# Kernel optimization log

Hardware: AMD Instinct MI355X
Metric: run time of the kernel (lower is better)

Reference implementation:

```python
import jax, jax.numpy as jnp
import numpy as np

H = 128  # hidden_size hard-coded in the torch module


def _lin(key, fan_in, shape):
    b = 1.0 / np.sqrt(fan_in)
    return jax.random.uniform(key, shape, minval=-b, maxval=b, dtype=jnp.float32)


def _gru_step(x, wih, bih, bhh):
    # torch GRU, single time step, h0 = 0; gate order (r, z, n)
    g = x @ wih.T + bih
    xr, xz, xn = jnp.split(g, 3, axis=-1)
    br, bz, bn = jnp.split(bhh, 3)
    r = jax.nn.sigmoid(xr + br)
    z = jax.nn.sigmoid(xz + bz)
    n = jnp.tanh(xn + r * bn)
    return (1.0 - z) * n  # h' = (1-z)*n + z*0


def _forward(x_node, x_edge, nt_w1, nt_b1, nt_w2, nt_b2, et_w, et_b,
             ngru_wih, ngru_bih, ngru_bhh, egru_wih, egru_bih, egru_bhh,
             natt_w, natt_b, eatt_w, eatt_b,
             lr_w1, lr_b1, lr_w2, lr_b2, cr_w1, cr_b1, cr_w2, cr_b2,
             mr_w1, mr_b1, mr_w2, mr_b2, pairs):
    B, N, _ = x_node.shape
    node_f = jax.nn.relu(x_node @ nt_w1 + nt_b1) @ nt_w2 + nt_b2      # [B,N,H]
    edge_f = x_edge @ et_w + et_b                                      # [B,N,N,H]
    nh = eh = None
    for _ in range(2):  # num_time_steps; GRU inputs are NOT updated in the original loop
        nh = _gru_step(node_f, ngru_wih, ngru_bih, ngru_bhh)           # [B,N,H]
        eh = _gru_step(edge_f, egru_wih, egru_bih, egru_bhh)           # [B,N,N,H]
        # --- node message pooling: attention over column index j ---
        n_col = jnp.broadcast_to(nh[:, :, None, :], eh.shape)          # aug[b,i,j] = nh[b,i]
        logits = (jnp.concatenate([n_col, eh], -1) @ natt_w)[..., 0] + natt_b[0]
        w = jax.nn.softmax(logits, axis=-1)                            # [B,N,N]
        nh = jnp.einsum('bijk,bij->bik', eh, w)                        # pooled node states
        # --- edge message pooling: 2-way attention over (row, col) node states ---
        n_row = jnp.broadcast_to(nh[:, None, :, :], eh.shape)          # [b,i,j] = nh[b,j]
        n_col = jnp.broadcast_to(nh[:, :, None, :], eh.shape)          # [b,i,j] = nh[b,i]
        l_row = (jnp.concatenate([n_row, eh], -1) @ eatt_w)[..., 0] + eatt_b[0]
        l_col = (jnp.concatenate([n_col, eh], -1) @ eatt_w)[..., 0] + eatt_b[0]
        w2 = jax.nn.softmax(jnp.stack([l_row, l_col], -1), axis=-1)    # [B,N,N,2]
        eh = w2[..., 0:1] * n_row + w2[..., 1:2] * n_col               # einsum('bijl,bijkl->bijk')
    # --- classifier inputs (aggregator = elementwise mean) ---
    i0, i1 = pairs[..., 0], pairs[..., 1]                              # [B,P]
    emb0 = jnp.take_along_axis(nh, i0[..., None], axis=1)              # [B,P,H]
    emb1 = jnp.take_along_axis(nh, i1[..., None], axis=1)
    bix = jnp.arange(B)[:, None]
    e01 = eh[bix, i0, i1]                                              # [B,P,H]
    e10 = eh[bix, i1, i0]
    ci = jnp.concatenate([(emb0 + emb1) * 0.5, (e01 + e10) * 0.5], -1)  # [B,P,2H]

    def head(w1, b1, wo, bo):
        return jax.nn.relu(ci @ w1 + b1) @ wo + bo

    lr = head(lr_w1, lr_b1, lr_w2, lr_b2)
    cr = head(cr_w1, cr_b1, cr_w2, cr_b2)
    mr = head(mr_w1, mr_b1, mr_w2, mr_b2)
    return jnp.concatenate([lr, cr, mr], axis=-1)                      # [B,P,6+5+3]


def setup_inputs() -> dict:
    B, N, P = 16, 64, 128
    NF, EF = 1024, 512
    CH = 512  # classifier hidden
    ks = list(jax.random.split(jax.random.key(0), 40))
    k = iter(ks)
    inp = {}
    inp['concatenated_node_features'] = jax.random.normal(next(k), (B, N, NF), dtype=jnp.float32)
    inp['interaction_feature'] = jax.random.normal(next(k), (B, N, N, EF), dtype=jnp.float32)
    inp['nt_w1'] = _lin(next(k), NF, (NF, 512)); inp['nt_b1'] = _lin(next(k), NF, (512,))
    inp['nt_w2'] = _lin(next(k), 512, (512, H)); inp['nt_b2'] = _lin(next(k), 512, (H,))
    inp['et_w'] = _lin(next(k), EF, (EF, H)); inp['et_b'] = _lin(next(k), EF, (H,))
    inp['ngru_wih'] = _lin(next(k), H, (3 * H, H))
    inp['ngru_bih'] = _lin(next(k), H, (3 * H,)); inp['ngru_bhh'] = _lin(next(k), H, (3 * H,))
    inp['egru_wih'] = _lin(next(k), H, (3 * H, H))
    inp['egru_bih'] = _lin(next(k), H, (3 * H,)); inp['egru_bhh'] = _lin(next(k), H, (3 * H,))
    inp['natt_w'] = _lin(next(k), 2 * H, (2 * H, 1)); inp['natt_b'] = _lin(next(k), 2 * H, (1,))
    inp['eatt_w'] = _lin(next(k), 2 * H, (2 * H, 1)); inp['eatt_b'] = _lin(next(k), 2 * H, (1,))
    for name, od in (('lr', 6), ('cr', 5), ('mr', 3)):
        inp[name + '_w1'] = _lin(next(k), 2 * H, (2 * H, CH))
        inp[name + '_b1'] = _lin(next(k), 2 * H, (CH,))
        inp[name + '_w2'] = _lin(next(k), CH, (CH, od))
        inp[name + '_b2'] = _lin(next(k), CH, (od,))
    inp['object_pairs'] = jax.random.randint(next(k), (B, P, 2), 0, N, dtype=jnp.int64 if jax.config.jax_enable_x64 else jnp.int32)
    inp['num_relation'] = jax.random.randint(next(k), (B,), 0, P, dtype=jnp.int64 if jax.config.jax_enable_x64 else jnp.int32)
    return inp


def reference(concatenated_node_features, interaction_feature,
              nt_w1, nt_b1, nt_w2, nt_b2, et_w, et_b,
              ngru_wih, ngru_bih, ngru_bhh, egru_wih, egru_bih, egru_bhh,
              natt_w, natt_b, eatt_w, eatt_b,
              lr_w1, lr_b1, lr_w2, lr_b2, cr_w1, cr_b1, cr_w2, cr_b2,
              mr_w1, mr_b1, mr_w2, mr_b2, object_pairs, num_relation):
    # num_relation is read but unused in the original make_classifier_inputs loop
    return _forward(concatenated_node_features, interaction_feature,
                    nt_w1, nt_b1, nt_w2, nt_b2, et_w, et_b,
                    ngru_wih, ngru_bih, ngru_bhh, egru_wih, egru_bih, egru_bhh,
                    natt_w, natt_b, eatt_w, eatt_b,
                    lr_w1, lr_b1, lr_w2, lr_b2, cr_w1, cr_b1, cr_w2, cr_b2,
                    mr_w1, mr_b1, mr_w2, mr_b2, object_pairs)
```

## Files before the change

### kernel.cpp

```cpp
#include <hip/hip_runtime.h>
#include <math.h>
#include <stdint.h>


typedef __attribute__((ext_vector_type(8))) short short8;
typedef __attribute__((ext_vector_type(4))) float f32x4;

#define DEVINL __device__ __forceinline__

DEVINL float sigmoidf_(float x) { return 1.0f / (1.0f + __expf(-x)); }
DEVINL float tanhf_(float x) {
    float e = __expf(2.0f * x);
    return (e - 1.0f) / (e + 1.0f);
}
DEVINL short bf16_rne(float f) {
    uint32_t u = __float_as_uint(f);
    u += 0x7FFFu + ((u >> 16) & 1u);
    return (short)(u >> 16);
}
DEVINL float bf16_to_f(short s) {
    return __uint_as_float(((uint32_t)(uint16_t)s) << 16);
}
DEVINL void gload_lds16(const void* g, void* l) {
    __builtin_amdgcn_global_load_lds(
        (const __attribute__((address_space(1))) void*)(uintptr_t)g,
        (__attribute__((address_space(3))) void*)(uint32_t)(uintptr_t)l,
        16, 0, 0);
}

__global__ __launch_bounds__(256) void prep_all(
    const float* __restrict__ et_w, const float* __restrict__ wih,
    const float* __restrict__ w1a, const float* __restrict__ w1b,
    const float* __restrict__ w1c,
    short* __restrict__ Bf1, short* __restrict__ Bf2,
    short* __restrict__ Wf1_hi, short* __restrict__ Wf1_lo)
{
    const int bid = blockIdx.x, t = threadIdx.x;
    if (bid < 256) {
        int idx = bid * 256 + t;
        int k = idx >> 7, n = idx & 127;
        float v = et_w[(size_t)k * 128 + n];
        short hi = bf16_rne(v), lo = bf16_rne(v - bf16_to_f(hi));
        int kt = k >> 5, ct = n >> 4;
        int lane = (((k >> 3) & 3) << 4) | (n & 15);
        int j = k & 7;
        size_t s0 = ((((size_t)kt * 2 + 0) * 8 + ct) * 64 + lane) * 8 + j;
        size_t s1 = ((((size_t)kt * 2 + 1) * 8 + ct) * 64 + lane) * 8 + j;
        Bf1[s0] = hi; Bf1[s1] = lo;
    } else if (bid < 448) {
        int idx = (bid - 256) * 256 + t;
        int n = idx >> 7, k = idx & 127;
        float v = wih[(size_t)n * 128 + k];
        short hi = bf16_rne(v), lo = bf16_rne(v - bf16_to_f(hi));
        int kt = k >> 5, ct = n >> 4;
        int lane = (((k >> 3) & 3) << 4) | (n & 15);
        int j = k & 7;
        size_t s0 = ((((size_t)kt * 2 + 0) * 24 + ct) * 64 + lane) * 8 + j;
        size_t s1 = ((((size_t)kt * 2 + 1) * 24 + ct) * 64 + lane) * 8 + j;
        Bf2[s0] = hi; Bf2[s1] = lo;
    } else {
        int idx = (bid - 448) * 256 + t;
        int h = idx >> 17;
        int r = idx & 131071;
        int k = r >> 9, c = r & 511;
        const float* w1 = (h == 0) ? w1a : (h == 1) ? w1b : w1c;
        float v = w1[(size_t)k * 512 + c];
        short hi = bf16_rne(v), lo = bf16_rne(v - bf16_to_f(hi));
        int kt = k >> 5, ct = c >> 4;
        int lane = (((k >> 3) & 3) << 4) | (c & 15);
        int j = k & 7;
        size_t fidx = ((((size_t)h * 8 + kt) * 32 + ct) * 64 + lane) * 8 + j;
        Wf1_hi[fidx] = hi;
        Wf1_lo[fidx] = lo;
    }
}

__global__ __launch_bounds__(256, 2) void fused_kernel(
    const float* __restrict__ x_edge,
    const short* __restrict__ Bf1, const short* __restrict__ Bf2,
    const float* __restrict__ et_b,
    const float* __restrict__ bih, const float* __restrict__ bhh,
    const float* __restrict__ natt_w, const float* __restrict__ eatt_w,
    float* __restrict__ nh_p, float* __restrict__ u_out)
{
    __shared__ __align__(16) char smem[81920];
    const int t = threadIdx.x;
    const int wv = t >> 6, lane = t & 63;
    const int g = blockIdx.x;
    const size_t bm = (size_t)g * 64;

    const int arow = t >> 2, akb = t & 3;
    const int aslotb = (((arow >> 4) * 64) + ((akb << 4) | (arow & 15))) * 16;
    const float* aptr = x_edge + (bm + arow) * 512 + akb * 8;

    f32x4 acc1[4][2] = {};

    {
        const char* src = (const char*)Bf1;
#pragma unroll
        for (int i = 0; i < 4; ++i) {
            int off = (t + i * 256) * 16;
            gload_lds16(src + off, smem + off);
        }
        float4 a0 = *(const float4*)(aptr);
        float4 a1 = *(const float4*)(aptr + 4);
        float av[8] = {a0.x, a0.y, a0.z, a0.w, a1.x, a1.y, a1.z, a1.w};
        short8 h8, l8;
#pragma unroll
        for (int j = 0; j < 8; ++j) {
            short h = bf16_rne(av[j]);
            h8[j] = h;
            l8[j] = bf16_rne(av[j] - bf16_to_f(h));
        }
        *(short8*)(smem + 32768 + aslotb) = h8;
        *(short8*)(smem + 32768 + 4096 + aslotb) = l8;
    }
    __syncthreads();

    for (int kt = 0; kt < 16; ++kt) {
        const int cur = kt & 1;
        float4 a0, a1;
        if (kt < 15) {
            const char* src = (const char*)Bf1 + (size_t)(kt + 1) * 16384;
            char* dst = smem + (cur ^ 1) * 16384;
#pragma unroll
            for (int i = 0; i < 4; ++i) {
                int off = (t + i * 256) * 16;
                gload_lds16(src + off, dst + off);
            }
            a0 = *(const float4*)(aptr + (size_t)(kt + 1) * 32);
            a1 = *(const float4*)(aptr + (size_t)(kt + 1) * 32 + 4);
        }

        const char* Bb = smem + cur * 16384;
        const char* Ah_c = smem + 32768 + cur * 8192;
        const char* Al_c = Ah_c + 4096;

        short8 Ahf[4], Alf[4];
#pragma unroll
        for (int rt = 0; rt < 4; ++rt) {
            Ahf[rt] = *(const short8*)(Ah_c + (rt * 64 + lane) * 16);
            Alf[rt] = *(const short8*)(Al_c + (rt * 64 + lane) * 16);
        }
#pragma unroll
        for (int c = 0; c < 2; ++c) {
            int ct = wv * 2 + c;
            short8 Bh = *(const short8*)(Bb + (ct * 64 + lane) * 16);
            short8 Bl = *(const short8*)(Bb + 8192 + (ct * 64 + lane) * 16);
#pragma unroll
            for (int rt = 0; rt < 4; ++rt) {
                acc1[rt][c] = __builtin_amdgcn_mfma_f32_16x16x32_bf16(Ahf[rt], Bh, acc1[rt][c], 0, 0, 0);
                acc1[rt][c] = __builtin_amdgcn_mfma_f32_16x16x32_bf16(Alf[rt], Bh, acc1[rt][c], 0, 0, 0);
                acc1[rt][c] = __builtin_amdgcn_mfma_f32_16x16x32_bf16(Ahf[rt], Bl, acc1[rt][c], 0, 0, 0);
            }
        }

        if (kt < 15) {
            float av[8] = {a0.x, a0.y, a0.z, a0.w, a1.x, a1.y, a1.z, a1.w};
            short8 h8, l8;
#pragma unroll
            for (int j = 0; j < 8; ++j) {
                short h = bf16_rne(av[j]);
                h8[j] = h;
                l8[j] = bf16_rne(av[j] - bf16_to_f(h));
            }
            char* dAh = smem + 32768 + (cur ^ 1) * 8192;
            *(short8*)(dAh + aslotb) = h8;
            *(short8*)(dAh + 4096 + aslotb) = l8;
        }
        __syncthreads();
    }

    float* ef_s = (float*)smem;
#pragma unroll
    for (int c = 0; c < 2; ++c) {
        int col = wv * 32 + c * 16 + (lane & 15);
        float bias = et_b[col];
#pragma unroll
        for (int rt = 0; rt < 4; ++rt) {
#pragma unroll
            for (int q = 0; q < 4; ++q) {
                int row = rt * 16 + ((lane >> 4) << 2) + q;
                ef_s[row * 132 + col] = acc1[rt][c][q] + bias;
            }
        }
    }
    __syncthreads();

    short* AF = (short*)(smem + 49152);
#pragma unroll
    for (int u2 = 0; u2 < 4; ++u2) {
        int unit = t + u2 * 256;
        int kt2 = unit >> 8;
        int rt = (unit >> 6) & 3;
        int ln = unit & 63;
        int row = rt * 16 + (ln & 15);
        int feat0 = kt2 * 32 + (ln >> 4) * 8;
        const float* src = ef_s + row * 132 + feat0;
        float4 v0 = *(const float4*)(src);
        float4 v1 = *(const float4*)(src + 4);
        float av[8] = {v0.x, v0.y, v0.z, v0.w, v1.x, v1.y, v1.z, v1.w};
        short8 h8, l8;
#pragma unroll
        for (int j = 0; j < 8; ++j) {
            short hh = bf16_rne(av[j]);
            h8[j] = hh;
            l8[j] = bf16_rne(av[j] - bf16_to_f(hh));
        }
        *(short8*)(AF + (((kt2 * 2 + 0) * 4 + rt) * 64 + ln) * 8) = h8;
        *(short8*)(AF + (((kt2 * 2 + 1) * 4 + rt) * 64 + ln) * 8) = l8;
    }
    __syncthreads();

    f32x4 acc[4][6] = {};
    for (int kt = 0; kt < 4; ++kt) {
        {
            const char* src = (const char*)Bf2 + (size_t)kt * 49152;
#pragma unroll
            for (int i = 0; i < 12; ++i) {
                int off = (t + i * 256) * 16;
                gload_lds16(src + off, smem + off);
            }
        }
        __syncthreads();

        const char* Ab = (const char*)AF + kt * 8192;
        short8 Ahf[4], Alf[4];
#pragma unroll
        for (int rt = 0; rt < 4; ++rt) {
            Ahf[rt] = *(const short8*)(Ab + (rt * 64 + lane) * 16);
            Alf[rt] = *(const short8*)(Ab + 4096 + (rt * 64 + lane) * 16);
        }
#pragma unroll
        for (int c = 0; c < 6; ++c) {
            int ctg = ((c >> 1) << 3) + (wv << 1) + (c & 1);
            short8 Bh = *(const short8*)(smem + (ctg * 64 + lane) * 16);
            short8 Bl = *(const short8*)(smem + 24576 + (ctg * 64 + lane) * 16);
#pragma unroll
            for (int rt = 0; rt < 4; ++rt) {
                acc[rt][c] = __builtin_amdgcn_mfma_f32_16x16x32_bf16(Ahf[rt], Bh, acc[rt][c], 0, 0, 0);
                acc[rt][c] = __builtin_amdgcn_mfma_f32_16x16x32_bf16(Alf[rt], Bh, acc[rt][c], 0, 0, 0);
                acc[rt][c] = __builtin_amdgcn_mfma_f32_16x16x32_bf16(Ahf[rt], Bl, acc[rt][c], 0, 0, 0);
            }
        }
        __syncthreads();
    }

    const int EHP = 132;
    float* eh_s = (float*)smem;
    float* red  = (float*)(smem + 33792);
    float* s2v  = red + 256;
    float* ewv  = s2v + 64;
#pragma unroll
    for (int cc = 0; cc < 2; ++cc) {
        int o = (wv << 5) + (cc << 4) + (lane & 15);
        float bco = bih[o] + bhh[o];
        float bcz = bih[128 + o] + bhh[128 + o];
        float bcn = bih[256 + o];
        float bn3 = bhh[256 + o];
#pragma unroll
        for (int rt = 0; rt < 4; ++rt) {
#pragma unroll
            for (int q = 0; q < 4; ++q) {
                int row = rt * 16 + ((lane >> 4) << 2) + q;
                float r = sigmoidf_(acc[rt][cc][q] + bco);
                float z = sigmoidf_(acc[rt][2 + cc][q] + bcz);
                float n = tanhf_(acc[rt][4 + cc][q] + bcn + r * bn3);
                eh_s[row * EHP + o] = (1.0f - z) * n;
            }
        }
    }
    __syncthreads();

    {
        int j = t >> 2, q = t & 3;
        const float* row = eh_s + j * EHP + q * 32;
        const float* wb = natt_w + 128 + q * 32;
        float a = 0.f;
#pragma unroll
        for (int k2 = 0; k2 < 32; ++k2) a = fmaf(row[k2], wb[k2], a);
        red[t] = a;
    }
    __syncthreads();
    if (t < 64) s2v[t] = red[4 * t] + red[4 * t + 1] + red[4 * t + 2] + red[4 * t + 3];
    __syncthreads();
    if (t < 64) {
        float m = -1e30f;
        for (int j = 0; j < 64; ++j) m = fmaxf(m, s2v[j]);
        ewv[t] = __expf(s2v[t] - m);
    }
    __syncthreads();
    float inv = 0.f;
    for (int j = 0; j < 64; ++j) inv += ewv[j];
    inv = 1.0f / inv;
    {
        int o = t & 127, h = t >> 7;
        float a = 0.f;
        for (int j = h * 32; j < h * 32 + 32; ++j)
            a = fmaf(ewv[j], eh_s[j * EHP + o], a);
        __syncthreads();
        red[t] = a;
    }
    __syncthreads();
    if (t < 128) {
        float v = (red[t] + red[t + 128]) * inv;
        nh_p[(size_t)g * 128 + t] = v;
        red[t] = v * eatt_w[t];
    }
    __syncthreads();
    for (int s = 64; s > 0; s >>= 1) {
        if (t < s) red[t] += red[t + s];
        __syncthreads();
    }
    if (t == 0) u_out[g] = red[0];
}

__global__ __launch_bounds__(128) void ci_kernel(
    const float* __restrict__ nh_p, const float* __restrict__ u,
    const int* __restrict__ pairs, float* __restrict__ ci)
{
    const int bp = blockIdx.x;
    const int b  = bp >> 7;
    const int t  = threadIdx.x;
    int i0 = pairs[bp * 2 + 0];
    int i1 = pairs[bp * 2 + 1];
    const float* n0 = nh_p + (size_t)(b * 64 + i0) * 128;
    const float* n1 = nh_p + (size_t)(b * 64 + i1) * 128;
    float s = sigmoidf_(u[b * 64 + i1] - u[b * 64 + i0]);
    float v0 = n0[t], v1 = n1[t];
    ci[(size_t)bp * 256 + t]       = 0.5f * (v0 + v1);
    ci[(size_t)bp * 256 + 128 + t] = s * v1 + (1.0f - s) * v0;
}

__global__ __launch_bounds__(256, 1) void headcls_kernel(
    const float* __restrict__ ci,
    const short* __restrict__ Wf1_hi, const short* __restrict__ Wf1_lo,
    const float* __restrict__ b1a, const float* __restrict__ b1b,
    const float* __restrict__ b1c,
    const float* __restrict__ w2a, const float* __restrict__ w2b,
    const float* __restrict__ w2c,
    const float* __restrict__ b2a, const float* __restrict__ b2b,
    const float* __restrict__ b2c,
    float* __restrict__ out)
{
    __shared__ __align__(16) char smem[139264];
    const int t = threadIdx.x;
    const int wv = t >> 6, lane = t & 63;
    const int rb = blockIdx.x;
    const int hd = blockIdx.y;
    const float* b1 = hd == 0 ? b1a : hd == 1 ? b1b : b1c;
    const float* w2 = hd == 0 ? w2a : hd == 1 ? w2b : w2c;
    const float* b2 = hd == 0 ? b2a : hd == 1 ? b2b : b2c;
    const int od  = hd == 0 ? 6 : hd == 1 ? 5 : 3;
    const int off = hd == 0 ? 0 : hd == 1 ? 6 : 11;

    const int arow = t >> 2, akb = t & 3;
    const int abyte = ((((arow >> 4) * 64) + ((akb << 4) | (arow & 15))) * 8) * 2;
    const float* aptr = ci + ((size_t)rb * 32 + arow) * 256 + akb * 8;

    f32x4 acc[2][8] = {};

    float4 a0, a1;
    if (t < 128) {
        a0 = *(const float4*)(aptr);
        a1 = *(const float4*)(aptr + 4);
    }
    {
        const char* sh = (const char*)(Wf1_hi + (size_t)hd * 8 * 32 * 512);
        const char* sl = (const char*)(Wf1_lo + (size_t)hd * 8 * 32 * 512);
#pragma unroll
        for (int i = 0; i < 8; ++i) {
            int ch = i * 4 + wv;
            int o2 = ch * 1024 + lane * 16;
            gload_lds16(sh + o2, smem + ch * 1024);
            gload_lds16(sl + o2, smem + 32768 + ch * 1024);
        }
    }
    if (t < 128) {
        float av[8] = {a0.x, a0.y, a0.z, a0.w, a1.x, a1.y, a1.z, a1.w};
        short8 h8, l8;
#pragma unroll
        for (int j = 0; j < 8; ++j) {
            short h = bf16_rne(av[j]);
            h8[j] = h;
            l8[j] = bf16_rne(av[j] - bf16_to_f(h));
        }
        *(short8*)(smem + 131072 + abyte) = h8;
        *(short8*)(smem + 131072 + 2048 + abyte) = l8;
    }
    __syncthreads();

    for (int kt = 0; kt < 8; ++kt) {
        const int cur = kt & 1;
        const char* Bh_c = smem + cur * 65536;
        const char* Bl_c = Bh_c + 32768;
        const char* Ah_c = smem + 131072 + cur * 4096;
        const char* Al_c = Ah_c + 2048;

        float4 b0, b1v;
        if (kt < 7) {
            const char* sh = (const char*)(Wf1_hi + ((size_t)hd * 8 + kt + 1) * 32 * 512);
            const char* sl = (const char*)(Wf1_lo + ((size_t)hd * 8 + kt + 1) * 32 * 512);
            char* dBh = smem + (cur ^ 1) * 65536;
#pragma unroll
            for (int i = 0; i < 8; ++i) {
                int ch = i * 4 + wv;
                int o2 = ch * 1024 + lane * 16;
                gload_lds16(sh + o2, dBh + ch * 1024);
                gload_lds16(sl + o2, dBh + 32768 + ch * 1024);
            }
            if (t < 128) {
                b0  = *(const float4*)(aptr + (size_t)(kt + 1) * 32);
                b1v = *(const float4*)(aptr + (size_t)(kt + 1) * 32 + 4);
            }
        }

        short8 Ah[2], Al[2];
#pragma unroll
        for (int rt = 0; rt < 2; ++rt) {
            Ah[rt] = *(const short8*)(Ah_c + (rt * 64 + lane) * 16);
            Al[rt] = *(const short8*)(Al_c + (rt * 64 + lane) * 16);
        }
#pragma unroll
        for (int c = 0; c < 8; ++c) {
            int ctg = wv * 8 + c;
            short8 Bh = *(const short8*)(Bh_c + (ctg * 64 + lane) * 16);
            short8 Bl = *(const short8*)(Bl_c + (ctg * 64 + lane) * 16);
#pragma unroll
            for (int rt = 0; rt < 2; ++rt) {
                acc[rt][c] = __builtin_amdgcn_mfma_f32_16x16x32_bf16(Ah[rt], Bh, acc[rt][c], 0, 0, 0);
                acc[rt][c] = __builtin_amdgcn_mfma_f32_16x16x32_bf16(Al[rt], Bh, acc[rt][c], 0, 0, 0);
                acc[rt][c] = __builtin_amdgcn_mfma_f32_16x16x32_bf16(Ah[rt], Bl, acc[rt][c], 0, 0, 0);
            }
        }

        if (kt < 7 && t < 128) {
            float av[8] = {b0.x, b0.y, b0.z, b0.w, b1v.x, b1v.y, b1v.z, b1v.w};
            short8 h8, l8;
#pragma unroll
            for (int j = 0; j < 8; ++j) {
                short h = bf16_rne(av[j]);
                h8[j] = h;
                l8[j] = bf16_rne(av[j] - bf16_to_f(h));
            }
            char* dAh = smem + 131072 + (cur ^ 1) * 4096;
            *(short8*)(dAh + abyte) = h8;
            *(short8*)(dAh + 2048 + abyte) = l8;
        }
        __syncthreads();
    }

    float* h_s  = (float*)smem;
    float* w2_s = (float*)(smem + 66048);
    for (int idx = t; idx < 512 * od; idx += 256) w2_s[idx] = w2[idx];
#pragma unroll
    for (int c = 0; c < 8; ++c) {
        int ctg = wv * 8 + c;
        int col = ctg * 16 + (lane & 15);
        float bias = b1[col];
#pragma unroll
        for (int rt = 0; rt < 2; ++rt) {
#pragma unroll
            for (int q = 0; q < 4; ++q) {
                int row = rt * 16 + ((lane >> 4) << 2) + q;
                h_s[row * 516 + col] = fmaxf(acc[rt][c][q] + bias, 0.f);
            }
        }
    }
    __syncthreads();

    {
        int row = t >> 3, o = t & 7;
        if (o < od) {
            const float* hr = h_s + row * 516;
            float a = b2[o];
            for (int c = 0; c < 512; ++c)
                a = fmaf(hr[c], w2_s[c * od + o], a);
            out[((size_t)rb * 32 + row) * 14 + off + o] = a;
        }
    }
}

extern "C" void kernel_launch(void* const* d_in, const int* in_sizes, int n_in,
                              void* d_out, int out_size, void* d_ws, size_t ws_size,
                              hipStream_t stream)
{
    const float* x_edge   = (const float*)d_in[1];
    const float* et_w     = (const float*)d_in[6];
    const float* et_b     = (const float*)d_in[7];
    const float* egru_wih = (const float*)d_in[11];
    const float* egru_bih = (const float*)d_in[12];
    const float* egru_bhh = (const float*)d_in[13];
    const float* natt_w   = (const float*)d_in[14];
    const float* eatt_w   = (const float*)d_in[16];
    const float* lr_w1 = (const float*)d_in[18];
    const float* lr_b1 = (const float*)d_in[19];
    const float* lr_w2 = (const float*)d_in[20];
    const float* lr_b2 = (const float*)d_in[21];
    const float* cr_w1 = (const float*)d_in[22];
    const float* cr_b1 = (const float*)d_in[23];
    const float* cr_w2 = (const float*)d_in[24];
    const float* cr_b2 = (const float*)d_in[25];
    const float* mr_w1 = (const float*)d_in[26];
    const float* mr_b1 = (const float*)d_in[27];
    const float* mr_w2 = (const float*)d_in[28];
    const float* mr_b2 = (const float*)d_in[29];
    const int* pairs   = (const int*)d_in[30];
    float* out = (float*)d_out;
    char* ws = (char*)d_ws;

    short* Bf1    = (short*)(ws + 0);
    short* Bf2    = (short*)(ws + 262144);
    short* Wf1_hi = (short*)(ws + 458752);
    short* Wf1_lo = (short*)(ws + 1245184);
    float* nh_p   = (float*)(ws + 2031616);
    float* u      = (float*)(ws + 2555904);
    float* ci     = (float*)(ws + 2560000);

    prep_all<<<1984, 256, 0, stream>>>(et_w, egru_wih, lr_w1, cr_w1, mr_w1,
                                       Bf1, Bf2, Wf1_hi, Wf1_lo);

    fused_kernel<<<1024, 256, 0, stream>>>(
        x_edge, Bf1, Bf2, et_b, egru_bih, egru_bhh, natt_w, eatt_w, nh_p, u);

    ci_kernel<<<2048, 128, 0, stream>>>(nh_p, u, pairs, ci);

    headcls_kernel<<<dim3(64, 3), 256, 0, stream>>>(
        ci, Wf1_hi, Wf1_lo, lr_b1, cr_b1, mr_b1,
        lr_w2, cr_w2, mr_w2, lr_b2, cr_b2, mr_b2, out);
}
```

Baseline: 100.9 us.

## Load B fragments directly into registers and deepen A prefetch in phase-1 GEMM

The first-phase edge-transform GEMM no longer stages the B operand (et_w split into hi/lo bf16) through LDS via global_load_lds. Each wave now loads its own B fragments straight into registers one k-tile ahead. The A tile prefetch is deepened to two k-tiles ahead using register ping-pong in a manually unrolled loop, and __syncthreads is replaced with a custom waitcnt+barrier. This cuts LDS traffic and buffer space, at the cost of more VGPRs and redundant global loads of B across blocks.

```diff
diff --git a/kernel.cpp b/kernel.cpp
--- a/kernel.cpp
+++ b/kernel.cpp
@@ -26,6 +26,10 @@
         (const __attribute__((address_space(1))) void*)(uintptr_t)g,
         (__attribute__((address_space(3))) void*)(uint32_t)(uintptr_t)l,
         16, 0, 0);
+}
+DEVINL void ldsbar() {
+    asm volatile("s_waitcnt lgkmcnt(0)\n\ts_barrier" ::: "memory");
+    __builtin_amdgcn_sched_barrier(0);
 }
 
 __global__ __launch_bounds__(256) void prep_all(
@@ -75,6 +79,49 @@
     }
 }
 
+#define PH1_ITER(KT, BH0, BH1, BL0, BL1, NBH0, NBH1, NBL0, NBL1,              \
+                 PCV0, PCV1, PLD0, PLD1, RBUF, WBUF)                          \
+    {                                                                         \
+        if ((KT) < 15) {                                                      \
+            const short* bkt = Bf1 + (size_t)((KT) + 1) * 8192;               \
+            NBH0 = *(const short8*)(bkt + ct0 * 512 + ln8);                   \
+            NBH1 = *(const short8*)(bkt + ct1 * 512 + ln8);                   \
+            NBL0 = *(const short8*)(bkt + 4096 + ct0 * 512 + ln8);            \
+            NBL1 = *(const short8*)(bkt + 4096 + ct1 * 512 + ln8);            \
+            float av[8] = {PCV0.x, PCV0.y, PCV0.z, PCV0.w,                    \
+                           PCV1.x, PCV1.y, PCV1.z, PCV1.w};                   \
+            short8 h8, l8;                                                    \
+            _Pragma("unroll") for (int j = 0; j < 8; ++j) {                   \
+                short h = bf16_rne(av[j]);                                    \
+                h8[j] = h;                                                    \
+                l8[j] = bf16_rne(av[j] - bf16_to_f(h));                       \
+            }                                                                 \
+            *(short8*)(smem + (WBUF) + aslotb) = h8;                          \
+            *(short8*)(smem + (WBUF) + 4096 + aslotb) = l8;                   \
+        }                                                                     \
+        if ((KT) < 14) {                                                      \
+            PLD0 = *(const float4*)(aptr + (size_t)((KT) + 2) * 32);          \
+            PLD1 = *(const float4*)(aptr + (size_t)((KT) + 2) * 32 + 4);      \
+        }                                                                     \
+        {                                                                     \
+            const char* Ah_c = smem + (RBUF);                                 \
+            short8 Ahf[4], Alf[4];                                            \
+            _Pragma("unroll") for (int rt = 0; rt < 4; ++rt) {                \
+                Ahf[rt] = *(const short8*)(Ah_c + (rt * 64 + lane) * 16);     \
+                Alf[rt] = *(const short8*)(Ah_c + 4096 + (rt * 64 + lane) * 16); \
+            }                                                                 \
+            _Pragma("unroll") for (int rt = 0; rt < 4; ++rt) {                \
+                acc1[rt][0] = __builtin_amdgcn_mfma_f32_16x16x32_bf16(Ahf[rt], BH0, acc1[rt][0], 0, 0, 0); \
+                acc1[rt][0] = __builtin_amdgcn_mfma_f32_16x16x32_bf16(Alf[rt], BH0, acc1[rt][0], 0, 0, 0); \
+                acc1[rt][0] = __builtin_amdgcn_mfma_f32_16x16x32_bf16(Ahf[rt], BL0, acc1[rt][0], 0, 0, 0); \
+                acc1[rt][1] = __builtin_amdgcn_mfma_f32_16x16x32_bf16(Ahf[rt], BH1, acc1[rt][1], 0, 0, 0); \
+                acc1[rt][1] = __builtin_amdgcn_mfma_f32_16x16x32_bf16(Alf[rt], BH1, acc1[rt][1], 0, 0, 0); \
+                acc1[rt][1] = __builtin_amdgcn_mfma_f32_16x16x32_bf16(Ahf[rt], BL1, acc1[rt][1], 0, 0, 0); \
+            }                                                                 \
+        }                                                                     \
+        ldsbar();                                                             \
+    }
+
 __global__ __launch_bounds__(256, 2) void fused_kernel(
     const float* __restrict__ x_edge,
     const short* __restrict__ Bf1, const short* __restrict__ Bf2,
@@ -93,18 +140,28 @@
     const int aslotb = (((arow >> 4) * 64) + ((akb << 4) | (arow & 15))) * 16;
     const float* aptr = x_edge + (bm + arow) * 512 + akb * 8;
 
+    const int ct0 = wv * 2, ct1 = wv * 2 + 1;
+    const int ln8 = lane * 8;
+
     f32x4 acc1[4][2] = {};
 
+    float4 paA0, paA1, paB0, paB1;
+    short8 bhA0, bhA1, blA0, blA1, bhB0, bhB1, blB0, blB1;
+
+    paA0 = *(const float4*)(aptr);
+    paA1 = *(const float4*)(aptr + 4);
+    paB0 = *(const float4*)(aptr + 32);
+    paB1 = *(const float4*)(aptr + 36);
     {
-        const char* src = (const char*)Bf1;
-#pragma unroll
-        for (int i = 0; i < 4; ++i) {
-            int off = (t + i * 256) * 16;
-            gload_lds16(src + off, smem + off);
-        }
-        float4 a0 = *(const float4*)(aptr);
-        float4 a1 = *(const float4*)(aptr + 4);
-        float av[8] = {a0.x, a0.y, a0.z, a0.w, a1.x, a1.y, a1.z, a1.w};
+        const short* bkt = Bf1;
+        bhA0 = *(const short8*)(bkt + ct0 * 512 + ln8);
+        bhA1 = *(const short8*)(bkt + ct1 * 512 + ln8);
+        blA0 = *(const short8*)(bkt + 4096 + ct0 * 512 + ln8);
+        blA1 = *(const short8*)(bkt + 4096 + ct1 * 512 + ln8);
+    }
+    {
+        float av[8] = {paA0.x, paA0.y, paA0.z, paA0.w,
+                       paA1.x, paA1.y, paA1.z, paA1.w};
         short8 h8, l8;
 #pragma unroll
         for (int j = 0; j < 8; ++j) {
@@ -112,64 +169,18 @@
             h8[j] = h;
             l8[j] = bf16_rne(av[j] - bf16_to_f(h));
         }
-        *(short8*)(smem + 32768 + aslotb) = h8;
-        *(short8*)(smem + 32768 + 4096 + aslotb) = l8;
-    }
-    __syncthreads();
-
-    for (int kt = 0; kt < 16; ++kt) {
-        const int cur = kt & 1;
-        float4 a0, a1;
-        if (kt < 15) {
-            const char* src = (const char*)Bf1 + (size_t)(kt + 1) * 16384;
-            char* dst = smem + (cur ^ 1) * 16384;
-#pragma unroll
-            for (int i = 0; i < 4; ++i) {
-                int off = (t + i * 256) * 16;
-                gload_lds16(src + off, dst + off);
-            }
-            a0 = *(const float4*)(aptr + (size_t)(kt + 1) * 32);
-            a1 = *(const float4*)(aptr + (size_t)(kt + 1) * 32 + 4);
-        }
-
-        const char* Bb = smem + cur * 16384;
-        const char* Ah_c = smem + 32768 + cur * 8192;
-        const char* Al_c = Ah_c + 4096;
-
-        short8 Ahf[4], Alf[4];
-#pragma unroll
-        for (int rt = 0; rt < 4; ++rt) {
-            Ahf[rt] = *(const short8*)(Ah_c + (rt * 64 + lane) * 16);
-            Alf[rt] = *(const short8*)(Al_c + (rt * 64 + lane) * 16);
-        }
-#pragma unroll
-        for (int c = 0; c < 2; ++c) {
-            int ct = wv * 2 + c;
-            short8 Bh = *(const short8*)(Bb + (ct * 64 + lane) * 16);
-            short8 Bl = *(const short8*)(Bb + 8192 + (ct * 64 + lane) * 16);
-#pragma unroll
-            for (int rt = 0; rt < 4; ++rt) {
-                acc1[rt][c] = __builtin_amdgcn_mfma_f32_16x16x32_bf16(Ahf[rt], Bh, acc1[rt][c], 0, 0, 0);
-                acc1[rt][c] = __builtin_amdgcn_mfma_f32_16x16x32_bf16(Alf[rt], Bh, acc1[rt][c], 0, 0, 0);
-                acc1[rt][c] = __builtin_amdgcn_mfma_f32_16x16x32_bf16(Ahf[rt], Bl, acc1[rt][c], 0, 0, 0);
-            }
-        }
-
-        if (kt < 15) {
-            float av[8] = {a0.x, a0.y, a0.z, a0.w, a1.x, a1.y, a1.z, a1.w};
-            short8 h8, l8;
-#pragma unroll
-            for (int j = 0; j < 8; ++j) {
-                short h = bf16_rne(av[j]);
-                h8[j] = h;
-                l8[j] = bf16_rne(av[j] - bf16_to_f(h));
-            }
-            char* dAh = smem + 32768 + (cur ^ 1) * 8192;
-            *(short8*)(dAh + aslotb) = h8;
-            *(short8*)(dAh + 4096 + aslotb) = l8;
-        }
-        __syncthreads();
-    }
+        *(short8*)(smem + aslotb) = h8;
+        *(short8*)(smem + 4096 + aslotb) = l8;
+    }
+    ldsbar();
+
+    for (int kt = 0; kt < 16; kt += 2) {
+        PH1_ITER(kt, bhA0, bhA1, blA0, blA1, bhB0, bhB1, blB0, blB1,
+                 paB0, paB1, paA0, paA1, 0, 8192)
+        PH1_ITER(kt + 1, bhB0, bhB1, blB0, blB1, bhA0, bhA1, blA0, blA1,
+                 paA0, paA1, paB0, paB1, 8192, 0)
+    }
+    __syncthreads();
 
     float* ef_s = (float*)smem;
 #pragma unroll
```

New measurement: 93.33 us. -7.5%, faster.
